# Performance work log

Hardware: AMD Instinct MI355X
Metric: run time of the kernel (lower is better)

Reference implementation:

```python
import jax, jax.numpy as jnp
import numpy as np

H, W = 256, 832            # full-res organized point cloud (HEIGHT/WIDTH globals)
STRIDE_H, STRIDE_W = 2, 4  # stride_H_list[0], stride_W_list[0]
OUT_H, OUT_W = 128, 208    # out_H_list[0], out_W_list[0]
KH, KW = 12, 20            # layer0 kernel_size
K = 32                     # layer0 K_sample


def _sa_layer(pts, h_idx, w_idx, w1, b1, w2, b2, w3, b3):
    """PointNet SA: strided center selection, window KNN grouping, MLP, max-pool.
    pts: (B,H,W,3); h_idx/w_idx: (M,) full-res grid coords of selected centers.
    """
    B = pts.shape[0]
    pts_flat = pts.reshape(B, H * W, 3)
    center_idx = h_idx * W + w_idx                      # (M,)
    centers = pts_flat[:, center_idx]                   # (B,M,3)  fast_select gather
    # candidate window around each center (clipped at borders)
    dh = jnp.arange(KH) - KH // 2
    dw = jnp.arange(KW) - KW // 2
    cand_h = jnp.clip(h_idx[:, None] + dh, 0, H - 1)    # (M,KH)
    cand_w = jnp.clip(w_idx[:, None] + dw, 0, W - 1)    # (M,KW)
    cand_idx = (cand_h[:, :, None] * W + cand_w[:, None, :]).reshape(-1, KH * KW)  # (M,P)
    cand = pts_flat[:, cand_idx]                        # (B,M,P,3) irregular gather
    d2 = jnp.sum((cand - centers[:, :, None, :]) ** 2, axis=-1)  # (B,M,P)
    _, nn = jax.lax.top_k(-d2, K)                       # K nearest within window
    knn = jnp.take_along_axis(cand, nn[..., None], axis=2)       # (B,M,K,3)
    rel = knn - centers[:, :, None, :]                  # local coordinates
    h = jax.nn.relu(rel @ w1 + b1)                      # mlp [8,8,16]
    h = jax.nn.relu(h @ w2 + b2)
    h = jax.nn.relu(h @ w3 + b3)
    return centers, jnp.max(h, axis=2)                  # (B,M,3), (B,M,16)


def setup_inputs() -> dict:
    key = jax.random.key(0)
    ks = jax.random.split(key, 5)
    return {
        "pos1": jax.random.normal(ks[0], (2, H, W, 3), jnp.float32) * 5.0,
        "pos2": jax.random.normal(ks[1], (2, H, W, 3), jnp.float32) * 5.0,
        "w1": jax.random.normal(ks[2], (3, 8), jnp.float32) * 0.3,
        "b1": jnp.zeros((8,), jnp.float32),
        "w2": jax.random.normal(ks[3], (8, 8), jnp.float32) * 0.3,
        "b2": jnp.zeros((8,), jnp.float32),
        "w3": jax.random.normal(ks[4], (8, 16), jnp.float32) * 0.3,
        "b3": jnp.zeros((16,), jnp.float32),
    }


def reference(pos1, pos2, w1, b1, w2, b2, w3, b3):
    # get_selected_idx for level 0: strided grid subsampling
    h_idx = jnp.repeat(jnp.arange(OUT_H) * STRIDE_H, OUT_W)  # (M,)
    w_idx = jnp.tile(jnp.arange(OUT_W) * STRIDE_W, OUT_H)    # (M,)
    _, f1 = _sa_layer(pos1, h_idx, w_idx, w1, b1, w2, b2, w3, b3)
    _, f2 = _sa_layer(pos2, h_idx, w_idx, w1, b1, w2, b2, w3, b3)
    return jnp.concatenate([f1, f2], axis=-1)  # (B, OUT_H*OUT_W, 32)
```

## Files before the change

### kernel.cpp

```cpp
#include <hip/hip_runtime.h>
#include <hip/hip_bf16.h>

#define HH 256
#define WW 832
#define OHH 128
#define OWW 208
#define NCAND 240
#define MM (OHH*OWW)

typedef float v2f __attribute__((ext_vector_type(2)));

__device__ __forceinline__ int iclamp(int v, int lo, int hi) { return min(max(v, lo), hi); }
__device__ __forceinline__ int mbcnt2(unsigned long long m) {
    return __builtin_amdgcn_mbcnt_hi((unsigned)(m >> 32),
           __builtin_amdgcn_mbcnt_lo((unsigned)m, 0));
}
__device__ __forceinline__ v2f sxor(v2f v, int m) {
    v2f r; r.x = __shfl_xor(v.x, m); r.y = __shfl_xor(v.y, m); return r;
}

__global__ void __launch_bounds__(256) sa_fused(
    const float* __restrict__ pos1, const float* __restrict__ pos2,
    const float* __restrict__ w1, const float* __restrict__ b1,
    const float* __restrict__ w2, const float* __restrict__ b2,
    const float* __restrict__ w3, const float* __restrict__ b3,
    float* __restrict__ out)
{
    __shared__ v2f sW1p[3][4];
    __shared__ v2f sW2p[8][4];
    __shared__ v2f sW3p[8][8];
    __shared__ v2f sB1p[4], sB2p[4], sB3p[8];
    __shared__ float4 selRel[128];

    const int t = threadIdx.x;
    if (t < 12)              { int i = t >> 2,  op = t & 3;
        sW1p[i][op] = (v2f){w1[i*8 + 2*op], w1[i*8 + 2*op + 1]}; }
    if (t >= 16 && t < 48)   { int u = t - 16, i = u >> 2, op = u & 3;
        sW2p[i][op] = (v2f){w2[i*8 + 2*op], w2[i*8 + 2*op + 1]}; }
    if (t >= 64 && t < 128)  { int u = t - 64, i = u >> 3, op = u & 7;
        sW3p[i][op] = (v2f){w3[i*16 + 2*op], w3[i*16 + 2*op + 1]}; }
    if (t >= 128 && t < 132) { int u = t - 128; sB1p[u] = (v2f){b1[2*u], b1[2*u + 1]}; }
    if (t >= 132 && t < 136) { int u = t - 132; sB2p[u] = (v2f){b2[2*u], b2[2*u + 1]}; }
    if (t >= 136 && t < 144) { int u = t - 136; sB3p[u] = (v2f){b3[2*u], b3[2*u + 1]}; }
    __syncthreads();

    const int lane = t & 63;
    const int wid  = t >> 6;
    const int m    = blockIdx.x * 4 + wid;
    const int b    = blockIdx.y & 1;
    const int cl   = blockIdx.y >> 1;
    const float* __restrict__ base = (cl ? pos2 : pos1) + (size_t)b * (HH * WW * 3);

    const unsigned um = (unsigned)m;
    const int oh = (int)(um / OWW);
    const int ow = (int)(um - (unsigned)oh * OWW);
    const int h0 = oh * 2, w0 = ow * 4;

    const float cx = base[(h0 * WW + w0) * 3 + 0];
    const float cy = base[(h0 * WW + w0) * 3 + 1];
    const float cz = base[(h0 * WW + w0) * 3 + 2];

    int kh  = (lane * 3277) >> 14;
    int kwb = (lane - kh * 5) * 4;
    if (lane >= 60) { kh = 11; kwb = 0; }

    unsigned d2b[4];
    float rxv[4], ryv[4], rzv[4];
    const bool interior = ((unsigned)(oh - 3) <= 122u) && ((unsigned)(ow - 3) <= 202u);
    if (interior) {
        const float* p = base + ((h0 - 6 + kh) * WW + (w0 - 10 + kwb)) * 3;
        float2 Av = *(const float2*)(p);
        float4 Bv = *(const float4*)(p + 2);
        float4 Cv = *(const float4*)(p + 6);
        float2 Dv = *(const float2*)(p + 10);
        float px[4] = {Av.x, Bv.y, Cv.x, Cv.w};
        float py[4] = {Av.y, Bv.z, Cv.y, Dv.x};
        float pz[4] = {Bv.x, Bv.w, Cv.z, Dv.y};
        #pragma unroll
        for (int q = 0; q < 4; ++q) {
            float dx = __fsub_rn(px[q], cx);
            float dy = __fsub_rn(py[q], cy);
            float dz = __fsub_rn(pz[q], cz);
            rxv[q] = dx; ryv[q] = dy; rzv[q] = dz;
            d2b[q] = __float_as_uint(__fadd_rn(__fadd_rn(__fmul_rn(dx, dx), __fmul_rn(dy, dy)), __fmul_rn(dz, dz)));
        }
    } else {
        int chh = iclamp(h0 - 6 + kh, 0, HH - 1);
        #pragma unroll
        for (int q = 0; q < 4; ++q) {
            int cw = iclamp(w0 - 10 + kwb + q, 0, WW - 1);
            const float* p = base + (chh * WW + cw) * 3;
            float dx = __fsub_rn(p[0], cx);
            float dy = __fsub_rn(p[1], cy);
            float dz = __fsub_rn(p[2], cz);
            rxv[q] = dx; ryv[q] = dy; rzv[q] = dz;
            d2b[q] = __float_as_uint(__fadd_rn(__fadd_rn(__fmul_rn(dx, dx), __fmul_rn(dy, dy)), __fmul_rn(dz, dz)));
        }
    }
    if (lane >= 60) { d2b[0] = d2b[1] = d2b[2] = d2b[3] = 0xFFFFFFFFu; }

    unsigned T = 0; int c0 = 0; bool exact = false;
    for (int bpos = 30; bpos >= 0; --bpos) {
        unsigned Q = T | (1u << bpos);
        unsigned long long t0 = __ballot(d2b[0] < Q);
        unsigned long long t1 = __ballot(d2b[1] < Q);
        unsigned long long t2 = __ballot(d2b[2] < Q);
        unsigned long long t3 = __ballot(d2b[3] < Q);
        int c = __popcll(t0) + __popcll(t1) + __popcll(t2) + __popcll(t3);
        if (c == 32) { T = Q; c0 = 32; exact = true; break; }
        if (c < 32)  { T = Q; c0 = c; }
    }

    bool tie0 = false, tie1 = false, tie2 = false, tie3 = false;
    if (!exact) {
        const int r = 32 - c0;
        bool eq0 = (d2b[0] == T), eq1 = (d2b[1] == T), eq2 = (d2b[2] == T), eq3 = (d2b[3] == T);
        unsigned long long e0 = __ballot(eq0);
        unsigned long long e1 = __ballot(eq1);
        unsigned long long e2 = __ballot(eq2);
        unsigned long long e3 = __ballot(eq3);
        int SA = mbcnt2(e0) + mbcnt2(e1) + mbcnt2(e2) + mbcnt2(e3);
        int E1 = (int)eq0, E2 = E1 + (int)eq1, E3 = E2 + (int)eq2;
        tie0 = eq0 && (SA      < r);
        tie1 = eq1 && (SA + E1 < r);
        tie2 = eq2 && (SA + E2 < r);
        tie3 = eq3 && (SA + E3 < r);
    }

    {
        bool m0 = (d2b[0] < T) || tie0;
        bool m1 = (d2b[1] < T) || tie1;
        bool m2 = (d2b[2] < T) || tie2;
        bool m3 = (d2b[3] < T) || tie3;
        unsigned long long s0 = __ballot(m0);
        unsigned long long s1 = __ballot(m1);
        unsigned long long s2 = __ballot(m2);
        unsigned long long s3 = __ballot(m3);
        int p1 = __popcll(s0);
        int p2 = p1 + __popcll(s1);
        int p3 = p2 + __popcll(s2);
        int lb = wid * 32;
        if (m0) selRel[lb +      mbcnt2(s0)] = make_float4(rxv[0], ryv[0], rzv[0], 0.f);
        if (m1) selRel[lb + p1 + mbcnt2(s1)] = make_float4(rxv[1], ryv[1], rzv[1], 0.f);
        if (m2) selRel[lb + p2 + mbcnt2(s2)] = make_float4(rxv[2], ryv[2], rzv[2], 0.f);
        if (m3) selRel[lb + p3 + mbcnt2(s3)] = make_float4(rxv[3], ryv[3], rzv[3], 0.f);
    }
    asm volatile("s_waitcnt lgkmcnt(0)" ::: "memory");
    __builtin_amdgcn_sched_barrier(0);

    {
        float4 rel = selRel[wid * 32 + (lane & 31)];
        v2f rx2 = (v2f){rel.x, rel.x};
        v2f ry2 = (v2f){rel.y, rel.y};
        v2f rz2 = (v2f){rel.z, rel.z};

        v2f a1[4];
        #pragma unroll
        for (int op = 0; op < 4; ++op) {
            v2f a = sB1p[op];
            a = __builtin_elementwise_fma(rx2, sW1p[0][op], a);
            a = __builtin_elementwise_fma(ry2, sW1p[1][op], a);
            a = __builtin_elementwise_fma(rz2, sW1p[2][op], a);
            a1[op] = __builtin_elementwise_max(a, (v2f)(0.f));
        }
        v2f a2[4];
        #pragma unroll
        for (int op = 0; op < 4; ++op) a2[op] = sB2p[op];
        #pragma unroll
        for (int i = 0; i < 8; ++i) {
            float h = a1[i >> 1][i & 1];
            v2f hb = (v2f){h, h};
            #pragma unroll
            for (int op = 0; op < 4; ++op)
                a2[op] = __builtin_elementwise_fma(hb, sW2p[i][op], a2[op]);
        }
        #pragma unroll
        for (int op = 0; op < 4; ++op) a2[op] = __builtin_elementwise_max(a2[op], (v2f)(0.f));

        const int obp = (lane >> 5) << 2;
        v2f a3[4];
        #pragma unroll
        for (int op = 0; op < 4; ++op) a3[op] = sB3p[obp + op];
        #pragma unroll
        for (int i = 0; i < 8; ++i) {
            float h = a2[i >> 1][i & 1];
            v2f hb = (v2f){h, h};
            #pragma unroll
            for (int op = 0; op < 4; ++op)
                a3[op] = __builtin_elementwise_fma(hb, sW3p[i][obp + op], a3[op]);
        }

        #pragma unroll
        for (int step = 16; step >= 1; step >>= 1) {
            #pragma unroll
            for (int op = 0; op < 4; ++op)
                a3[op] = __builtin_elementwise_max(a3[op], sxor(a3[op], step));
        }
        if ((lane & 31) == 0) {
            #pragma unroll
            for (int op = 0; op < 4; ++op)
                a3[op] = __builtin_elementwise_max(a3[op], (v2f)(0.f));
            const int ob = (lane >> 5) << 3;
            float4* dst = (float4*)(out + ((size_t)(b * MM + m) * 32) + (size_t)cl * 16 + ob);
            dst[0] = make_float4(a3[0].x, a3[0].y, a3[1].x, a3[1].y);
            dst[1] = make_float4(a3[2].x, a3[2].y, a3[3].x, a3[3].y);
        }
    }
}

extern "C" void kernel_launch(void* const* d_in, const int* in_sizes, int n_in,
                              void* d_out, int out_size, void* d_ws, size_t ws_size,
                              hipStream_t stream) {
    const float* pos1 = (const float*)d_in[0];
    const float* pos2 = (const float*)d_in[1];
    const float* w1   = (const float*)d_in[2];
    const float* b1   = (const float*)d_in[3];
    const float* w2   = (const float*)d_in[4];
    const float* b2   = (const float*)d_in[5];
    const float* w3   = (const float*)d_in[6];
    const float* b3   = (const float*)d_in[7];
    float* out = (float*)d_out;

    dim3 grid(MM / 4, 4);
    sa_fused<<<grid, 256, 0, stream>>>(pos1, pos2, w1, b1, w2, b2, w3, b3, out);
}
```

Before: 94.95 us.

## Process two centers per wavefront and run full MLP per lane

```diff
diff --git a/kernel.cpp b/kernel.cpp
--- a/kernel.cpp
+++ b/kernel.cpp
@@ -18,6 +18,8 @@
 __device__ __forceinline__ v2f sxor(v2f v, int m) {
     v2f r; r.x = __shfl_xor(v.x, m); r.y = __shfl_xor(v.y, m); return r;
 }
+__device__ __forceinline__ v2f lo2(float4 f) { return (v2f){f.x, f.y}; }
+__device__ __forceinline__ v2f hi2(float4 f) { return (v2f){f.z, f.w}; }
 
 __global__ void __launch_bounds__(256) sa_fused(
     const float* __restrict__ pos1, const float* __restrict__ pos2,
@@ -26,184 +28,204 @@
     const float* __restrict__ w3, const float* __restrict__ b3,
     float* __restrict__ out)
 {
-    __shared__ v2f sW1p[3][4];
-    __shared__ v2f sW2p[8][4];
-    __shared__ v2f sW3p[8][8];
-    __shared__ v2f sB1p[4], sB2p[4], sB3p[8];
-    __shared__ float4 selRel[128];
+    __shared__ float4 sW1q[3][2];
+    __shared__ float4 sW2q[8][2];
+    __shared__ float4 sW3q[8][4];
+    __shared__ float4 sB1q[2], sB2q[2], sB3q[4];
+    __shared__ float4 selRel[256];
 
     const int t = threadIdx.x;
-    if (t < 12)              { int i = t >> 2,  op = t & 3;
-        sW1p[i][op] = (v2f){w1[i*8 + 2*op], w1[i*8 + 2*op + 1]}; }
-    if (t >= 16 && t < 48)   { int u = t - 16, i = u >> 2, op = u & 3;
-        sW2p[i][op] = (v2f){w2[i*8 + 2*op], w2[i*8 + 2*op + 1]}; }
-    if (t >= 64 && t < 128)  { int u = t - 64, i = u >> 3, op = u & 7;
-        sW3p[i][op] = (v2f){w3[i*16 + 2*op], w3[i*16 + 2*op + 1]}; }
-    if (t >= 128 && t < 132) { int u = t - 128; sB1p[u] = (v2f){b1[2*u], b1[2*u + 1]}; }
-    if (t >= 132 && t < 136) { int u = t - 132; sB2p[u] = (v2f){b2[2*u], b2[2*u + 1]}; }
-    if (t >= 136 && t < 144) { int u = t - 136; sB3p[u] = (v2f){b3[2*u], b3[2*u + 1]}; }
+    if (t < 6)            { int i = t >> 1, qd = (t & 1) * 4;
+        sW1q[i][t & 1] = make_float4(w1[i*8+qd], w1[i*8+qd+1], w1[i*8+qd+2], w1[i*8+qd+3]); }
+    if (t >= 8 && t < 24) { int u = t - 8, i = u >> 1, qd = (u & 1) * 4;
+        sW2q[i][u & 1] = make_float4(w2[i*8+qd], w2[i*8+qd+1], w2[i*8+qd+2], w2[i*8+qd+3]); }
+    if (t >= 32 && t < 64){ int u = t - 32, i = u >> 2, qd = (u & 3) * 4;
+        sW3q[i][u & 3] = make_float4(w3[i*16+qd], w3[i*16+qd+1], w3[i*16+qd+2], w3[i*16+qd+3]); }
+    if (t >= 64 && t < 66){ int u = (t - 64) * 4; sB1q[t-64] = make_float4(b1[u], b1[u+1], b1[u+2], b1[u+3]); }
+    if (t >= 66 && t < 68){ int u = (t - 66) * 4; sB2q[t-66] = make_float4(b2[u], b2[u+1], b2[u+2], b2[u+3]); }
+    if (t >= 68 && t < 72){ int u = (t - 68) * 4; sB3q[t-68] = make_float4(b3[u], b3[u+1], b3[u+2], b3[u+3]); }
     __syncthreads();
 
     const int lane = t & 63;
     const int wid  = t >> 6;
-    const int m    = blockIdx.x * 4 + wid;
+    const int l31  = lane & 31;
+    const int mA   = blockIdx.x * 8 + wid * 2;
     const int b    = blockIdx.y & 1;
     const int cl   = blockIdx.y >> 1;
     const float* __restrict__ base = (cl ? pos2 : pos1) + (size_t)b * (HH * WW * 3);
 
-    const unsigned um = (unsigned)m;
-    const int oh = (int)(um / OWW);
-    const int ow = (int)(um - (unsigned)oh * OWW);
-    const int h0 = oh * 2, w0 = ow * 4;
-
-    const float cx = base[(h0 * WW + w0) * 3 + 0];
-    const float cy = base[(h0 * WW + w0) * 3 + 1];
-    const float cz = base[(h0 * WW + w0) * 3 + 2];
-
     int kh  = (lane * 3277) >> 14;
     int kwb = (lane - kh * 5) * 4;
     if (lane >= 60) { kh = 11; kwb = 0; }
 
-    unsigned d2b[4];
-    float rxv[4], ryv[4], rzv[4];
-    const bool interior = ((unsigned)(oh - 3) <= 122u) && ((unsigned)(ow - 3) <= 202u);
-    if (interior) {
-        const float* p = base + ((h0 - 6 + kh) * WW + (w0 - 10 + kwb)) * 3;
-        float2 Av = *(const float2*)(p);
-        float4 Bv = *(const float4*)(p + 2);
-        float4 Cv = *(const float4*)(p + 6);
-        float2 Dv = *(const float2*)(p + 10);
-        float px[4] = {Av.x, Bv.y, Cv.x, Cv.w};
-        float py[4] = {Av.y, Bv.z, Cv.y, Dv.x};
-        float pz[4] = {Bv.x, Bv.w, Cv.z, Dv.y};
-        #pragma unroll
-        for (int q = 0; q < 4; ++q) {
-            float dx = __fsub_rn(px[q], cx);
-            float dy = __fsub_rn(py[q], cy);
-            float dz = __fsub_rn(pz[q], cz);
-            rxv[q] = dx; ryv[q] = dy; rzv[q] = dz;
-            d2b[q] = __float_as_uint(__fadd_rn(__fadd_rn(__fmul_rn(dx, dx), __fmul_rn(dy, dy)), __fmul_rn(dz, dz)));
-        }
-    } else {
-        int chh = iclamp(h0 - 6 + kh, 0, HH - 1);
-        #pragma unroll
-        for (int q = 0; q < 4; ++q) {
-            int cw = iclamp(w0 - 10 + kwb + q, 0, WW - 1);
-            const float* p = base + (chh * WW + cw) * 3;
-            float dx = __fsub_rn(p[0], cx);
-            float dy = __fsub_rn(p[1], cy);
-            float dz = __fsub_rn(p[2], cz);
-            rxv[q] = dx; ryv[q] = dy; rzv[q] = dz;
-            d2b[q] = __float_as_uint(__fadd_rn(__fadd_rn(__fmul_rn(dx, dx), __fmul_rn(dy, dy)), __fmul_rn(dz, dz)));
-        }
-    }
-    if (lane >= 60) { d2b[0] = d2b[1] = d2b[2] = d2b[3] = 0xFFFFFFFFu; }
-
-    unsigned T = 0; int c0 = 0; bool exact = false;
-    for (int bpos = 30; bpos >= 0; --bpos) {
-        unsigned Q = T | (1u << bpos);
-        unsigned long long t0 = __ballot(d2b[0] < Q);
-        unsigned long long t1 = __ballot(d2b[1] < Q);
-        unsigned long long t2 = __ballot(d2b[2] < Q);
-        unsigned long long t3 = __ballot(d2b[3] < Q);
-        int c = __popcll(t0) + __popcll(t1) + __popcll(t2) + __popcll(t3);
-        if (c == 32) { T = Q; c0 = 32; exact = true; break; }
-        if (c < 32)  { T = Q; c0 = c; }
-    }
-
-    bool tie0 = false, tie1 = false, tie2 = false, tie3 = false;
-    if (!exact) {
-        const int r = 32 - c0;
-        bool eq0 = (d2b[0] == T), eq1 = (d2b[1] == T), eq2 = (d2b[2] == T), eq3 = (d2b[3] == T);
-        unsigned long long e0 = __ballot(eq0);
-        unsigned long long e1 = __ballot(eq1);
-        unsigned long long e2 = __ballot(eq2);
-        unsigned long long e3 = __ballot(eq3);
-        int SA = mbcnt2(e0) + mbcnt2(e1) + mbcnt2(e2) + mbcnt2(e3);
-        int E1 = (int)eq0, E2 = E1 + (int)eq1, E3 = E2 + (int)eq2;
-        tie0 = eq0 && (SA      < r);
-        tie1 = eq1 && (SA + E1 < r);
-        tie2 = eq2 && (SA + E2 < r);
-        tie3 = eq3 && (SA + E3 < r);
-    }
-
-    {
-        bool m0 = (d2b[0] < T) || tie0;
-        bool m1 = (d2b[1] < T) || tie1;
-        bool m2 = (d2b[2] < T) || tie2;
-        bool m3 = (d2b[3] < T) || tie3;
-        unsigned long long s0 = __ballot(m0);
-        unsigned long long s1 = __ballot(m1);
-        unsigned long long s2 = __ballot(m2);
-        unsigned long long s3 = __ballot(m3);
-        int p1 = __popcll(s0);
-        int p2 = p1 + __popcll(s1);
-        int p3 = p2 + __popcll(s2);
-        int lb = wid * 32;
-        if (m0) selRel[lb +      mbcnt2(s0)] = make_float4(rxv[0], ryv[0], rzv[0], 0.f);
-        if (m1) selRel[lb + p1 + mbcnt2(s1)] = make_float4(rxv[1], ryv[1], rzv[1], 0.f);
-        if (m2) selRel[lb + p2 + mbcnt2(s2)] = make_float4(rxv[2], ryv[2], rzv[2], 0.f);
-        if (m3) selRel[lb + p3 + mbcnt2(s3)] = make_float4(rxv[3], ryv[3], rzv[3], 0.f);
+    #pragma unroll
+    for (int cc = 0; cc < 2; ++cc) {
+        const int m  = mA + cc;
+        const int oh = (int)(((unsigned)(m >> 4) * 5042u) >> 16);
+        const int ow = m - oh * OWW;
+        const int h0 = oh * 2, w0 = ow * 4;
+
+        const float cx = base[(h0 * WW + w0) * 3 + 0];
+        const float cy = base[(h0 * WW + w0) * 3 + 1];
+        const float cz = base[(h0 * WW + w0) * 3 + 2];
+
+        unsigned d2b[4];
+        float rxv[4], ryv[4], rzv[4];
+        const bool interior = ((unsigned)(oh - 3) <= 122u) && ((unsigned)(ow - 3) <= 202u);
+        if (interior) {
+            const float* p = base + ((h0 - 6 + kh) * WW + (w0 - 10 + kwb)) * 3;
+            float2 Av = *(const float2*)(p);
+            float4 Bv = *(const float4*)(p + 2);
+            float4 Cv = *(const float4*)(p + 6);
+            float2 Dv = *(const float2*)(p + 10);
+            float px[4] = {Av.x, Bv.y, Cv.x, Cv.w};
+            float py[4] = {Av.y, Bv.z, Cv.y, Dv.x};
+            float pz[4] = {Bv.x, Bv.w, Cv.z, Dv.y};
+            #pragma unroll
+            for (int q = 0; q < 4; ++q) {
+                float dx = __fsub_rn(px[q], cx);
+                float dy = __fsub_rn(py[q], cy);
+                float dz = __fsub_rn(pz[q], cz);
+                rxv[q] = dx; ryv[q] = dy; rzv[q] = dz;
+                d2b[q] = __float_as_uint(__fadd_rn(__fadd_rn(__fmul_rn(dx, dx), __fmul_rn(dy, dy)), __fmul_rn(dz, dz)));
+            }
+        } else {
+            int chh = iclamp(h0 - 6 + kh, 0, HH - 1);
+            #pragma unroll
+            for (int q = 0; q < 4; ++q) {
+                int cw = iclamp(w0 - 10 + kwb + q, 0, WW - 1);
+                const float* p = base + (chh * WW + cw) * 3;
+                float dx = __fsub_rn(p[0], cx);
+                float dy = __fsub_rn(p[1], cy);
+                float dz = __fsub_rn(p[2], cz);
+                rxv[q] = dx; ryv[q] = dy; rzv[q] = dz;
+                d2b[q] = __float_as_uint(__fadd_rn(__fadd_rn(__fmul_rn(dx, dx), __fmul_rn(dy, dy)), __fmul_rn(dz, dz)));
+            }
+        }
+        if (lane >= 60) { d2b[0] = d2b[1] = d2b[2] = d2b[3] = 0xFFFFFFFFu; }
+
+        unsigned T = 0; int c0 = 0; bool exact = false;
+        unsigned long long sv0 = 0, sv1 = 0, sv2 = 0, sv3 = 0;
+        for (int bpos = 30; bpos >= 0; --bpos) {
+            unsigned Q = T | (1u << bpos);
+            unsigned long long t0 = __ballot(d2b[0] < Q);
+            unsigned long long t1 = __ballot(d2b[1] < Q);
+            unsigned long long t2 = __ballot(d2b[2] < Q);
+            unsigned long long t3 = __ballot(d2b[3] < Q);
+            int c = __popcll(t0) + __popcll(t1) + __popcll(t2) + __popcll(t3);
+            if (c == 32) { T = Q; exact = true; sv0 = t0; sv1 = t1; sv2 = t2; sv3 = t3; break; }
+            if (c < 32)  { T = Q; c0 = c; }
+        }
+
+        bool m0, m1, m2, m3;
+        unsigned long long s0, s1, s2, s3;
+        if (exact) {
+            m0 = (d2b[0] < T); m1 = (d2b[1] < T); m2 = (d2b[2] < T); m3 = (d2b[3] < T);
+            s0 = sv0; s1 = sv1; s2 = sv2; s3 = sv3;
+        } else {
+            const int r = 32 - c0;
+            bool eq0 = (d2b[0] == T), eq1 = (d2b[1] == T), eq2 = (d2b[2] == T), eq3 = (d2b[3] == T);
+            unsigned long long e0 = __ballot(eq0);
+            unsigned long long e1 = __ballot(eq1);
+            unsigned long long e2 = __ballot(eq2);
+            unsigned long long e3 = __ballot(eq3);
+            int SA = mbcnt2(e0) + mbcnt2(e1) + mbcnt2(e2) + mbcnt2(e3);
+            int E1 = (int)eq0, E2 = E1 + (int)eq1, E3 = E2 + (int)eq2;
+            m0 = (d2b[0] < T) || (eq0 && (SA      < r));
+            m1 = (d2b[1] < T) || (eq1 && (SA + E1 < r));
+            m2 = (d2b[2] < T) || (eq2 && (SA + E2 < r));
+            m3 = (d2b[3] < T) || (eq3 && (SA + E3 < r));
+            s0 = __ballot(m0); s1 = __ballot(m1); s2 = __ballot(m2); s3 = __ballot(m3);
+        }
+
+        {
+            int p1 = __popcll(s0);
+            int p2 = p1 + __popcll(s1);
+            int p3 = p2 + __popcll(s2);
+            int lb = wid * 64 + cc * 32;
+            if (m0) selRel[lb +      mbcnt2(s0)] = make_float4(rxv[0], ryv[0], rzv[0], 0.f);
+            if (m1) selRel[lb + p1 + mbcnt2(s1)] = make_float4(rxv[1], ryv[1], rzv[1], 0.f);
+            if (m2) selRel[lb + p2 + mbcnt2(s2)] = make_float4(rxv[2], ryv[2], rzv[2], 0.f);
+            if (m3) selRel[lb + p3 + mbcnt2(s3)] = make_float4(rxv[3], ryv[3], rzv[3], 0.f);
+        }
     }
     asm volatile("s_waitcnt lgkmcnt(0)" ::: "memory");
     __builtin_amdgcn_sched_barrier(0);
 
     {
-        float4 rel = selRel[wid * 32 + (lane & 31)];
+        float4 rel = selRel[wid * 64 + lane];
         v2f rx2 = (v2f){rel.x, rel.x};
         v2f ry2 = (v2f){rel.y, rel.y};
         v2f rz2 = (v2f){rel.z, rel.z};
 
         v2f a1[4];
-        #pragma unroll
-        for (int op = 0; op < 4; ++op) {
-            v2f a = sB1p[op];
-            a = __builtin_elementwise_fma(rx2, sW1p[0][op], a);
-            a = __builtin_elementwise_fma(ry2, sW1p[1][op], a);
-            a = __builtin_elementwise_fma(rz2, sW1p[2][op], a);
-            a1[op] = __builtin_elementwise_max(a, (v2f)(0.f));
-        }
-        v2f a2[4];
-        #pragma unroll
-        for (int op = 0; op < 4; ++op) a2[op] = sB2p[op];
+        {
+            float4 bq0 = sB1q[0], bq1 = sB1q[1];
+            float4 x0 = sW1q[0][0], x1 = sW1q[0][1];
+            float4 y0 = sW1q[1][0], y1 = sW1q[1][1];
+            float4 z0 = sW1q[2][0], z1 = sW1q[2][1];
+            a1[0] = __builtin_elementwise_fma(rx2, lo2(x0), lo2(bq0));
+            a1[1] = __builtin_elementwise_fma(rx2, hi2(x0), hi2(bq0));
+            a1[2] = __builtin_elementwise_fma(rx2, lo2(x1), lo2(bq1));
+            a1[3] = __builtin_elementwise_fma(rx2, hi2(x1), hi2(bq1));
+            a1[0] = __builtin_elementwise_fma(ry2, lo2(y0), a1[0]);
+            a1[1] = __builtin_elementwise_fma(ry2, hi2(y0), a1[1]);
+            a1[2] = __builtin_elementwise_fma(ry2, lo2(y1), a1[2]);
+            a1[3] = __builtin_elementwise_fma(ry2, hi2(y1), a1[3]);
+            a1[0] = __builtin_elementwise_fma(rz2, lo2(z0), a1[0]);
+            a1[1] = __builtin_elementwise_fma(rz2, hi2(z0), a1[1]);
+            a1[2] = __builtin_elementwise_fma(rz2, lo2(z1), a1[2]);
+            a1[3] = __builtin_elementwise_fma(rz2, hi2(z1), a1[3]);
+            #pragma unroll
+            for (int op = 0; op < 4; ++op) a1[op] = __builtin_elementwise_max(a1[op], (v2f)(0.f));
+        }
+        v2f a2[4] = {lo2(sB2q[0]), hi2(sB2q[0]), lo2(sB2q[1]), hi2(sB2q[1])};
         #pragma unroll
         for (int i = 0; i < 8; ++i) {
             float h = a1[i >> 1][i & 1];
             v2f hb = (v2f){h, h};
-            #pragma unroll
-            for (int op = 0; op < 4; ++op)
-                a2[op] = __builtin_elementwise_fma(hb, sW2p[i][op], a2[op]);
+            float4 wl = sW2q[i][0], wh = sW2q[i][1];
+            a2[0] = __builtin_elementwise_fma(hb, lo2(wl), a2[0]);
+            a2[1] = __builtin_elementwise_fma(hb, hi2(wl), a2[1]);
+            a2[2] = __builtin_elementwise_fma(hb, lo2(wh), a2[2]);
+            a2[3] = __builtin_elementwise_fma(hb, hi2(wh), a2[3]);
         }
         #pragma unroll
         for (int op = 0; op < 4; ++op) a2[op] = __builtin_elementwise_max(a2[op], (v2f)(0.f));
 
-        const int obp = (lane >> 5) << 2;
-        v2f a3[4];
-        #pragma unroll
-        for (int op = 0; op < 4; ++op) a3[op] = sB3p[obp + op];
+        v2f a3[8] = {lo2(sB3q[0]), hi2(sB3q[0]), lo2(sB3q[1]), hi2(sB3q[1]),
+                     lo2(sB3q[2]), hi2(sB3q[2]), lo2(sB3q[3]), hi2(sB3q[3])};
         #pragma unroll
         for (int i = 0; i < 8; ++i) {
             float h = a2[i >> 1][i & 1];
             v2f hb = (v2f){h, h};
-            #pragma unroll
-            for (int op = 0; op < 4; ++op)
-                a3[op] = __builtin_elementwise_fma(hb, sW3p[i][obp + op], a3[op]);
+            float4 q0 = sW3q[i][0], q1 = sW3q[i][1], q2 = sW3q[i][2], q3 = sW3q[i][3];
+            a3[0] = __builtin_elementwise_fma(hb, lo2(q0), a3[0]);
+            a3[1] = __builtin_elementwise_fma(hb, hi2(q0), a3[1]);
+            a3[2] = __builtin_elementwise_fma(hb, lo2(q1), a3[2]);
+            a3[3] = __builtin_elementwise_fma(hb, hi2(q1), a3[3]);
+            a3[4] = __builtin_elementwise_fma(hb, lo2(q2), a3[4]);
+            a3[5] = __builtin_elementwise_fma(hb, hi2(q2), a3[5]);
+            a3[6] = __builtin_elementwise_fma(hb, lo2(q3), a3[6]);
+            a3[7] = __builtin_elementwise_fma(hb, hi2(q3), a3[7]);
         }
 
         #pragma unroll
         for (int step = 16; step >= 1; step >>= 1) {
             #pragma unroll
-            for (int op = 0; op < 4; ++op)
+            for (int op = 0; op < 8; ++op)
                 a3[op] = __builtin_elementwise_max(a3[op], sxor(a3[op], step));
         }
-        if ((lane & 31) == 0) {
-            #pragma unroll
-            for (int op = 0; op < 4; ++op)
+        if (l31 == 0) {
+            #pragma unroll
+            for (int op = 0; op < 8; ++op)
                 a3[op] = __builtin_elementwise_max(a3[op], (v2f)(0.f));
-            const int ob = (lane >> 5) << 3;
-            float4* dst = (float4*)(out + ((size_t)(b * MM + m) * 32) + (size_t)cl * 16 + ob);
+            const int ms = mA + (lane >> 5);
+            float4* dst = (float4*)(out + ((size_t)(b * MM + ms) * 32) + (size_t)cl * 16);
             dst[0] = make_float4(a3[0].x, a3[0].y, a3[1].x, a3[1].y);
             dst[1] = make_float4(a3[2].x, a3[2].y, a3[3].x, a3[3].y);
+            dst[2] = make_float4(a3[4].x, a3[4].y, a3[5].x, a3[5].y);
+            dst[3] = make_float4(a3[6].x, a3[6].y, a3[7].x, a3[7].y);
         }
     }
 }
@@ -221,6 +243,6 @@
     const float* b3   = (const float*)d_in[7];
     float* out = (float*)d_out;
 
-    dim3 grid(MM / 4, 4);
+    dim3 grid(MM / 8, 4);
     sa_fused<<<grid, 256, 0, stream>>>(pos1, pos2, w1, b1, w2, b2, w3, b3, out);
 }
```

Result: faster. 88.45 us (-6.8%).
